# Performance work log

Hardware: AMD Instinct MI355X
Metric: run time of the kernel (lower is better)

## Reference

```python
import jax, jax.numpy as jnp
import numpy as np

HEADS = 8


def _attn_1d(xs, w_qkv, w_proj, heads, scale):
    """xs: [N, C, L] -> [N, C, L]. 1x1 conv == channel matmul."""
    n, c, l = xs.shape
    inner = w_proj.shape[1]
    d = inner // heads
    qkv = jnp.einsum('oc,ncl->nol', w_qkv, xs)          # [N, 3*inner, L]
    q, k, v = jnp.split(qkv, 3, axis=1)                  # each [N, inner, L]
    # [N, heads, L, d]
    q = q.reshape(n, heads, d, l).transpose(0, 1, 3, 2)
    k = k.reshape(n, heads, d, l).transpose(0, 1, 3, 2)
    v = v.reshape(n, heads, d, l).transpose(0, 1, 3, 2)
    attn = jax.nn.softmax(jnp.einsum('nhid,nhjd->nhij', q, k) * scale, axis=-1)
    out = jnp.einsum('nhij,nhjd->nhid', attn, v)         # [N, heads, L, d]
    out = out.transpose(0, 1, 3, 2).reshape(n, inner, l) # [N, inner, L]
    return jnp.einsum('co,nol->ncl', w_proj, out)


def _axial(x, w_qkv, w_proj, heads, scale, axis):
    b, c, h, w = x.shape
    if axis == 'h':
        xs = x.transpose(0, 3, 1, 2).reshape(b * w, c, h)
        out = _attn_1d(xs, w_qkv, w_proj, heads, scale)
        return out.reshape(b, w, c, h).transpose(0, 2, 3, 1)
    else:
        xs = x.transpose(0, 2, 1, 3).reshape(b * h, c, w)
        out = _attn_1d(xs, w_qkv, w_proj, heads, scale)
        return out.reshape(b, h, c, w).transpose(0, 2, 1, 3)


def setup_inputs() -> dict:
    key = jax.random.key(0)
    k1, k2, k3 = jax.random.split(key, 3)
    B, C, H, W = 4, 512, 128, 128
    heads = HEADS
    head_dim = C // heads
    inner = head_dim * heads
    x = jax.random.normal(k1, (B, C, H, W), dtype=jnp.float32)
    w_qkv = jax.random.normal(k2, (inner * 3, C), dtype=jnp.float32) * 0.02
    w_proj = jax.random.normal(k3, (C, inner), dtype=jnp.float32) * 0.02
    return {"x": x, "w_qkv": w_qkv, "w_proj": w_proj}


def reference(x, w_qkv, w_proj):
    c = x.shape[1]
    head_dim = c // HEADS
    scale = head_dim ** (-0.5)
    h_out = _axial(x, w_qkv, w_proj, HEADS, scale, 'h')
    w_out = _axial(h_out, w_qkv, w_proj, HEADS, scale, 'w')
    return x + w_out
```

## Files before the change

### kernel.cpp

```cpp
#include <hip/hip_runtime.h>
#include <hip/hip_bf16.h>
#include <stdint.h>

#define B_ 4
#define S_ 128
#define CH 512

typedef __attribute__((ext_vector_type(8))) __bf16 bf16x8;
typedef __attribute__((ext_vector_type(4))) float  f32x4;
typedef __attribute__((ext_vector_type(16))) float f32x16;

__device__ __forceinline__ unsigned short f2b(float f) {
    union { float f; unsigned u; } v; v.f = f;
    unsigned r = v.u + 0x7FFFu + ((v.u >> 16) & 1u);
    return (unsigned short)(r >> 16);
}

#define GLD_LDS16(gp, lp) \
    __builtin_amdgcn_global_load_lds((const __attribute__((address_space(1))) void*)(gp), \
                                     (__attribute__((address_space(3))) void*)(lp), 16, 0, 0)

__global__ void cvt_w(const float* __restrict__ wq, const float* __restrict__ wp,
                      unsigned short* __restrict__ wqb, unsigned short* __restrict__ wpb) {
    int idx = (blockIdx.x * 256 + threadIdx.x) * 4;
    const float* s; unsigned short* d; int off;
    if (idx < 1536 * 512) { s = wq; d = wqb; off = idx; }
    else                  { s = wp; d = wpb; off = idx - 1536 * 512; }
    float4 v = *(const float4*)(s + off);
    ushort4 o; o.x = f2b(v.x); o.y = f2b(v.y); o.z = f2b(v.z); o.w = f2b(v.w);
    *(ushort4*)(d + off) = o;
}

__global__ __launch_bounds__(256) void k0_tr(const float* __restrict__ x,
                                             unsigned short* __restrict__ xb) {
    __shared__ unsigned short t[64][72];
    int bid = blockIdx.x;
    int ct = bid & 7, wt = (bid >> 3) & 1, h = (bid >> 4) & 127, b = bid >> 11;
    int tid = threadIdx.x;
    int c0 = ct * 64, w0 = wt * 64;
    const float* xp = x + ((size_t)b * CH * S_ + h) * S_;
    int wl = (tid & 15) * 4;
#pragma unroll
    for (int it = 0; it < 4; ++it) {
        int c = it * 16 + (tid >> 4);
        float4 v = *(const float4*)(xp + (size_t)(c0 + c) * (S_ * S_) + w0 + wl);
        t[wl + 0][c] = f2b(v.x);
        t[wl + 1][c] = f2b(v.y);
        t[wl + 2][c] = f2b(v.z);
        t[wl + 3][c] = f2b(v.w);
    }
    __syncthreads();
#pragma unroll
    for (int it = 0; it < 2; ++it) {
        int w = it * 32 + (tid >> 3);
        int ce = (tid & 7) * 8;
        int4 v = *(const int4*)&t[w][ce];
        size_t p = (size_t)((b * 128 + w0 + w) * 128 + h);
        *(int4*)(xb + p * 512 + c0 + ce) = v;
    }
}

template<int EPI>
__global__ __launch_bounds__(512, 2) void gemm8(
    const unsigned short* __restrict__ A,
    const unsigned short* __restrict__ Bm,
    unsigned short* __restrict__ outb,
    const float* __restrict__ xres,
    float* __restrict__ outf,
    int Mtiles)
{
    __shared__ unsigned short lds[65536];
    const int NT = 8;
    int nwg = gridDim.x;
    int wg = (blockIdx.x & 7) * (nwg >> 3) + (blockIdx.x >> 3);
    int mb = wg % Mtiles, nb = wg / Mtiles;
    int m0 = mb * 256, n0 = nb * 256;
    int tid = threadIdx.x, lane = tid & 63, wid = tid >> 6;
    int wm = wid >> 2, wn = wid & 3;

    f32x16 acc[4][2] = {};

    int l31  = lane & 31;
    int rsw  = ((lane >> 2) & 3) << 4;
    int cK[4];
#pragma unroll
    for (int ks = 0; ks < 4; ++ks)
        cK[ks] = (ks * 16 + (lane >> 5) * 8) ^ rsw;
    int arow0 = (wm * 64 + l31) * 64;
    int brow  = (wn * 32 + l31) * 64;

    int srow = tid >> 3;
    int scol = ((tid & 7) * 8) ^ (((srow >> 2) & 3) << 4);
    const unsigned short* Ab0 = A  + (size_t)(m0 + srow) * 512 + scol;
    const unsigned short* Bb0 = Bm + (size_t)(n0 + (srow >> 5) * 64 + (srow & 31)) * 512 + scol;

#define STAGE_A(kt, reg) do {                                                  \
        unsigned short* lb_ = &lds[((((kt) & 1) * 2 + (reg)) * 8192)];         \
        const unsigned short* g_ = Ab0 + (size_t)(reg) * (64 * 512) + (kt) * 64;\
        GLD_LDS16(g_,             lb_ + wid * 512);                            \
        GLD_LDS16(g_ + 128 * 512, lb_ + 4096 + wid * 512);                     \
    } while (0)
#define STAGE_B(kt, reg) do {                                                  \
        unsigned short* lb_ = &lds[32768 + ((((kt) & 1) * 2 + (reg)) * 8192)]; \
        const unsigned short* g_ = Bb0 + (size_t)(reg) * (32 * 512) + (kt) * 64;\
        GLD_LDS16(g_,             lb_ + wid * 512);                            \
        GLD_LDS16(g_ + 128 * 512, lb_ + 4096 + wid * 512);                     \
    } while (0)

    STAGE_A(0, 0); STAGE_A(0, 1); STAGE_B(0, 0); STAGE_B(0, 1);
    STAGE_A(1, 0); STAGE_B(1, 0);
    asm volatile("s_waitcnt vmcnt(4)" ::: "memory");
    __builtin_amdgcn_s_barrier();

    for (int j = 0; j < NT; ++j) {
        int db = j & 1;
        bf16x8 af[2][4];
#pragma unroll
        for (int q = 0; q < 4; ++q) {
            const int mq = q >> 1, nq = q & 1;
            int bbase = 32768 + (db * 2 + nq) * 8192 + brow;
            if (nq == 0) {
                int abase = (db * 2 + mq) * 8192 + arow0;
#pragma unroll
                for (int fr = 0; fr < 2; ++fr)
#pragma unroll
                    for (int ks = 0; ks < 4; ++ks)
                        af[fr][ks] = *(const bf16x8*)&lds[abase + fr * 2048 + cK[ks]];
            }
            bf16x8 bq[4];
#pragma unroll
            for (int ks = 0; ks < 4; ++ks)
                bq[ks] = *(const bf16x8*)&lds[bbase + cK[ks]];
            if (q == 0)      { if (j + 1 < NT) STAGE_A(j + 1, 1); }
            else if (q == 1) { if (j + 1 < NT) STAGE_B(j + 1, 1); }
            else if (q == 2) { if (j + 2 < NT) STAGE_A(j + 2, 0); }
            else {
                if (j + 2 < NT) STAGE_B(j + 2, 0);
                if (j < NT - 2) asm volatile("s_waitcnt vmcnt(4)" ::: "memory");
                else            asm volatile("s_waitcnt vmcnt(0)" ::: "memory");
            }
            __builtin_amdgcn_s_barrier();
            asm volatile("s_waitcnt lgkmcnt(0)" ::: "memory");
            __builtin_amdgcn_s_setprio(1);
#pragma unroll
            for (int ks = 0; ks < 4; ++ks)
#pragma unroll
                for (int fr = 0; fr < 2; ++fr)
                    acc[mq * 2 + fr][nq] = __builtin_amdgcn_mfma_f32_32x32x16_bf16(
                        af[fr][ks], bq[ks], acc[mq * 2 + fr][nq], 0, 0, 0);
            __builtin_amdgcn_s_setprio(0);
            __builtin_amdgcn_s_barrier();
        }
    }
#undef STAGE_A
#undef STAGE_B

#pragma unroll
    for (int mi2 = 0; mi2 < 4; ++mi2) {
#pragma unroll
        for (int qd = 0; qd < 4; ++qd) {
            int row0 = m0 + wm * 128 + mi2 * 32 + qd * 8 + ((lane >> 5) << 2);
#pragma unroll
            for (int nq = 0; nq < 2; ++nq) {
                int col = n0 + wn * 64 + nq * 32 + (lane & 31);
                int i = col & 127, sq = (col >> 7) & 127, bb = col >> 14;
                float a4[4];
#pragma unroll
                for (int r = 0; r < 4; ++r) a4[r] = acc[mi2][nq][qd * 4 + r];
                if (EPI == 0) {
                    int g = row0 >> 6, d0 = row0 & 63;
                    if (g < 16) {
                        size_t base = ((size_t)(g * 4 + bb) * 16384 + (size_t)sq * 128 + i) * 64 + d0;
                        ushort4 o;
                        o.x = f2b(a4[0]); o.y = f2b(a4[1]); o.z = f2b(a4[2]); o.w = f2b(a4[3]);
                        *(ushort4*)(outb + base) = o;
                    } else {
                        size_t base = ((size_t)(g * 4 + bb) * 8192 + (size_t)sq * 64 + d0) * 128 + i;
                        outb[base]       = f2b(a4[0]);
                        outb[base + 128] = f2b(a4[1]);
                        outb[base + 256] = f2b(a4[2]);
                        outb[base + 384] = f2b(a4[3]);
                    }
                } else if (EPI == 1) {
                    size_t p2 = ((size_t)bb * 128 + i) * 128 + sq;
                    ushort4 o;
                    o.x = f2b(a4[0]); o.y = f2b(a4[1]); o.z = f2b(a4[2]); o.w = f2b(a4[3]);
                    *(ushort4*)(outb + p2 * 512 + row0) = o;
                } else {
                    size_t base = (((size_t)bb * 512 + row0) * 128 + sq) * 128 + i;
#pragma unroll
                    for (int r = 0; r < 4; ++r) {
                        size_t a_ = base + (size_t)r * 16384;
                        outf[a_] = xres[a_] + a4[r];
                    }
                }
            }
        }
    }
}

__global__ __launch_bounds__(256) void attn_k(const unsigned short* __restrict__ qkv,
                                              unsigned short* __restrict__ o2) {
    __shared__ unsigned short Qs[128 * 80];
    __shared__ unsigned short Ks[128 * 80];
    __shared__ unsigned short Vt[64 * 144];
    int bid = blockIdx.x;
    int t = bid & 7, sq = (bid >> 3) & 127, b = bid >> 10;
    int tid = threadIdx.x, lane = tid & 63, wv = tid >> 6;
    const unsigned short* qg = qkv + ((size_t)(t * 4 + b) * 16384 + (size_t)sq * 128) * 64;
    const unsigned short* kg = qkv + ((size_t)((8 + t) * 4 + b) * 16384 + (size_t)sq * 128) * 64;
    const unsigned short* vg = qkv + ((size_t)((16 + t) * 4 + b) * 8192 + (size_t)sq * 64) * 128;
    {
        int r = tid >> 3, d0 = (tid & 7) * 8;
#pragma unroll
        for (int it = 0; it < 4; ++it) {
            *(int4*)(Qs + (it * 32 + r) * 80 + d0) = *(const int4*)(qg + (it * 32 + r) * 64 + d0);
            *(int4*)(Ks + (it * 32 + r) * 80 + d0) = *(const int4*)(kg + (it * 32 + r) * 64 + d0);
        }
        int r2 = tid >> 4, i0 = (tid & 15) * 8;
#pragma unroll
        for (int it = 0; it < 4; ++it)
            *(int4*)(Vt + (it * 16 + r2) * 144 + i0) = *(const int4*)(vg + (it * 16 + r2) * 128 + i0);
    }
    __syncthreads();

    f32x4 st[8][2] = {};
#pragma unroll
    for (int kk = 0; kk < 2; ++kk) {
        int ko = kk * 32 + (lane >> 4) * 8;
        bf16x8 bq[2];
#pragma unroll
        for (int nt = 0; nt < 2; ++nt)
            bq[nt] = *(const bf16x8*)(Qs + (wv * 32 + nt * 16 + (lane & 15)) * 80 + ko);
#pragma unroll
        for (int mt = 0; mt < 8; ++mt) {
            bf16x8 ak = *(const bf16x8*)(Ks + (mt * 16 + (lane & 15)) * 80 + ko);
#pragma unroll
            for (int nt = 0; nt < 2; ++nt)
                st[mt][nt] = __builtin_amdgcn_mfma_f32_16x16x32_bf16(ak, bq[nt], st[mt][nt], 0, 0, 0);
        }
    }

    const float sc = 0.125f * 1.44269504088896f;
    float mx[2], rinv[2];
    unsigned ppk[8][2][2];
#pragma unroll
    for (int nt = 0; nt < 2; ++nt) {
        float m = -3.0e38f;
#pragma unroll
        for (int mt = 0; mt < 8; ++mt)
#pragma unroll
            for (int r = 0; r < 4; ++r)
                m = fmaxf(m, st[mt][nt][r]);
        m = fmaxf(m, __shfl_xor(m, 16));
        m = fmaxf(m, __shfl_xor(m, 32));
        mx[nt] = m * sc;
    }
#pragma unroll
    for (int nt = 0; nt < 2; ++nt) {
        float s = 0.f;
#pragma unroll
        for (int mt = 0; mt < 8; ++mt) {
            float p0 = exp2f(st[mt][nt][0] * sc - mx[nt]);
            float p1 = exp2f(st[mt][nt][1] * sc - mx[nt]);
            float p2 = exp2f(st[mt][nt][2] * sc - mx[nt]);
            float p3 = exp2f(st[mt][nt][3] * sc - mx[nt]);
            s += (p0 + p1) + (p2 + p3);
            ppk[mt][nt][0] = (unsigned)f2b(p0) | ((unsigned)f2b(p1) << 16);
            ppk[mt][nt][1] = (unsigned)f2b(p2) | ((unsigned)f2b(p3) << 16);
        }
        s += __shfl_xor(s, 16);
        s += __shfl_xor(s, 32);
        rinv[nt] = 1.0f / s;
    }

    f32x4 ov[4][2] = {};
    int g = lane >> 4;
    int ls0 = (lane & 15) | ((g & 1) << 5);
    int ls1 = ls0 | 16;
    int hi = g >> 1;
#pragma unroll
    for (int kt = 0; kt < 4; ++kt) {
        bf16x8 bp[2];
#pragma unroll
        for (int nt = 0; nt < 2; ++nt) {
            unsigned a0 = (unsigned)__shfl((int)ppk[2 * kt    ][nt][0], ls0);
            unsigned b0 = (unsigned)__shfl((int)ppk[2 * kt + 1][nt][0], ls0);
            unsigned a1 = (unsigned)__shfl((int)ppk[2 * kt    ][nt][1], ls0);
            unsigned b1 = (unsigned)__shfl((int)ppk[2 * kt + 1][nt][1], ls0);
            unsigned a2 = (unsigned)__shfl((int)ppk[2 * kt    ][nt][0], ls1);
            unsigned b2 = (unsigned)__shfl((int)ppk[2 * kt + 1][nt][0], ls1);
            unsigned a3 = (unsigned)__shfl((int)ppk[2 * kt    ][nt][1], ls1);
            unsigned b3 = (unsigned)__shfl((int)ppk[2 * kt + 1][nt][1], ls1);
            union { unsigned u[4]; bf16x8 v; } pk;
            pk.u[0] = hi ? b0 : a0;
            pk.u[1] = hi ? b1 : a1;
            pk.u[2] = hi ? b2 : a2;
            pk.u[3] = hi ? b3 : a3;
            bp[nt] = pk.v;
        }
#pragma unroll
        for (int dt = 0; dt < 4; ++dt) {
            bf16x8 av = *(const bf16x8*)(Vt + (dt * 16 + (lane & 15)) * 144 + kt * 32 + (lane >> 4) * 8);
#pragma unroll
            for (int nt = 0; nt < 2; ++nt)
                ov[dt][nt] = __builtin_amdgcn_mfma_f32_16x16x32_bf16(av, bp[nt], ov[dt][nt], 0, 0, 0);
        }
    }

#pragma unroll
    for (int dt = 0; dt < 4; ++dt) {
        int d0 = dt * 16 + (lane >> 4) * 4;
#pragma unroll
        for (int nt = 0; nt < 2; ++nt) {
            int i = wv * 32 + nt * 16 + (lane & 15);
            size_t p = ((size_t)(b * 128 + sq)) * 128 + i;
            ushort4 o;
            o.x = f2b(ov[dt][nt][0] * rinv[nt]);
            o.y = f2b(ov[dt][nt][1] * rinv[nt]);
            o.z = f2b(ov[dt][nt][2] * rinv[nt]);
            o.w = f2b(ov[dt][nt][3] * rinv[nt]);
            *(ushort4*)(o2 + p * 512 + t * 64 + d0) = o;
        }
    }
}

extern "C" void kernel_launch(void* const* d_in, const int* in_sizes, int n_in,
                              void* d_out, int out_size, void* d_ws, size_t ws_size,
                              hipStream_t stream) {
    const float* x  = (const float*)d_in[0];
    const float* wq = (const float*)d_in[1];
    const float* wp = (const float*)d_in[2];
    float* out = (float*)d_out;
    char* ws = (char*)d_ws;
    unsigned short* wqb = (unsigned short*)(ws);
    unsigned short* wpb = (unsigned short*)(ws + ((size_t)2 << 20));
    unsigned short* xb  = (unsigned short*)(ws + ((size_t)4 << 20));
    unsigned short* o2  = (unsigned short*)(ws + ((size_t)68 << 20));
    unsigned short* qkv = (unsigned short*)(ws + ((size_t)132 << 20));

    cvt_w<<<1024, 256, 0, stream>>>(wq, wp, wqb, wpb);
    k0_tr<<<8192, 256, 0, stream>>>(x, xb);
    gemm8<0><<<6 * 256, 512, 0, stream>>>(wqb, xb, qkv, nullptr, nullptr, 6);
    attn_k<<<4096, 256, 0, stream>>>(qkv, o2);
    gemm8<1><<<2 * 256, 512, 0, stream>>>(wpb, o2, xb, nullptr, nullptr, 2);
    gemm8<0><<<6 * 256, 512, 0, stream>>>(wqb, xb, qkv, nullptr, nullptr, 6);
    attn_k<<<4096, 256, 0, stream>>>(qkv, o2);
    gemm8<2><<<2 * 256, 512, 0, stream>>>(wpb, o2, nullptr, x, out, 2);
}
```

Before: 589.2 us.

## Reschedule GEMM main loop quadrants to cut barriers and reorder B staging

Restructures the inner K-loop of the bf16 MFMA GEMM so each iteration walks the four quadrants in a snake order (00,01,11,10), reusing loaded A/B fragments across adjacent quadrants. It also changes which B half is prefetched when, and drops the per-quadrant barrier pairs and explicit lgkmcnt waits. The goal is to reduce synchronisation and LDS reload overhead and overlap the global-to-LDS prefetch with MFMA work better. Correctness now depends on the new staging order avoiding overwriting LDS buffers that other waves are still reading, and without explicit lgkmcnt waits it relies on the compiler to insert them.

```diff
diff --git a/kernel.cpp b/kernel.cpp
--- a/kernel.cpp
+++ b/kernel.cpp
@@ -107,51 +107,61 @@
         GLD_LDS16(g_ + 128 * 512, lb_ + 4096 + wid * 512);                     \
     } while (0)
 
+#define LOAD_AF(reg) do {                                                      \
+        int abase_ = (db * 2 + (reg)) * 8192 + arow0;                          \
+        _Pragma("unroll")                                                      \
+        for (int fr = 0; fr < 2; ++fr)                                         \
+            _Pragma("unroll")                                                  \
+            for (int ks = 0; ks < 4; ++ks)                                     \
+                af[fr][ks] = *(const bf16x8*)&lds[abase_ + fr * 2048 + cK[ks]];\
+    } while (0)
+#define LOAD_BQ(reg) do {                                                      \
+        int bbase_ = 32768 + (db * 2 + (reg)) * 8192 + brow;                   \
+        _Pragma("unroll")                                                      \
+        for (int ks = 0; ks < 4; ++ks)                                         \
+            bq[ks] = *(const bf16x8*)&lds[bbase_ + cK[ks]];                    \
+    } while (0)
+#define MFMA8(mq, nq)                                                          \
+    __builtin_amdgcn_s_setprio(1);                                             \
+    _Pragma("unroll")                                                          \
+    for (int ks = 0; ks < 4; ++ks)                                             \
+        _Pragma("unroll")                                                      \
+        for (int fr = 0; fr < 2; ++fr)                                         \
+            acc[(mq) * 2 + fr][nq] = __builtin_amdgcn_mfma_f32_32x32x16_bf16(  \
+                af[fr][ks], bq[ks], acc[(mq) * 2 + fr][nq], 0, 0, 0);          \
+    __builtin_amdgcn_s_setprio(0);
+
     STAGE_A(0, 0); STAGE_A(0, 1); STAGE_B(0, 0); STAGE_B(0, 1);
-    STAGE_A(1, 0); STAGE_B(1, 0);
+    STAGE_A(1, 0); STAGE_B(1, 1);
     asm volatile("s_waitcnt vmcnt(4)" ::: "memory");
     __builtin_amdgcn_s_barrier();
 
     for (int j = 0; j < NT; ++j) {
-        int db = j & 1;
-        bf16x8 af[2][4];
-#pragma unroll
-        for (int q = 0; q < 4; ++q) {
-            const int mq = q >> 1, nq = q & 1;
-            int bbase = 32768 + (db * 2 + nq) * 8192 + brow;
-            if (nq == 0) {
-                int abase = (db * 2 + mq) * 8192 + arow0;
-#pragma unroll
-                for (int fr = 0; fr < 2; ++fr)
-#pragma unroll
-                    for (int ks = 0; ks < 4; ++ks)
-                        af[fr][ks] = *(const bf16x8*)&lds[abase + fr * 2048 + cK[ks]];
-            }
-            bf16x8 bq[4];
-#pragma unroll
-            for (int ks = 0; ks < 4; ++ks)
-                bq[ks] = *(const bf16x8*)&lds[bbase + cK[ks]];
-            if (q == 0)      { if (j + 1 < NT) STAGE_A(j + 1, 1); }
-            else if (q == 1) { if (j + 1 < NT) STAGE_B(j + 1, 1); }
-            else if (q == 2) { if (j + 2 < NT) STAGE_A(j + 2, 0); }
-            else {
-                if (j + 2 < NT) STAGE_B(j + 2, 0);
-                if (j < NT - 2) asm volatile("s_waitcnt vmcnt(4)" ::: "memory");
-                else            asm volatile("s_waitcnt vmcnt(0)" ::: "memory");
-            }
-            __builtin_amdgcn_s_barrier();
-            asm volatile("s_waitcnt lgkmcnt(0)" ::: "memory");
-            __builtin_amdgcn_s_setprio(1);
-#pragma unroll
-            for (int ks = 0; ks < 4; ++ks)
-#pragma unroll
-                for (int fr = 0; fr < 2; ++fr)
-                    acc[mq * 2 + fr][nq] = __builtin_amdgcn_mfma_f32_32x32x16_bf16(
-                        af[fr][ks], bq[ks], acc[mq * 2 + fr][nq], 0, 0, 0);
-            __builtin_amdgcn_s_setprio(0);
-            __builtin_amdgcn_s_barrier();
-        }
-    }
+        const int db = j & 1;
+        bf16x8 af[2][4], bq[4];
+        LOAD_AF(0);
+        LOAD_BQ(0);
+        if (j + 1 < NT) STAGE_A(j + 1, 1);
+        MFMA8(0, 0)
+        LOAD_BQ(1);
+        if (j + 1 < NT) STAGE_B(j + 1, 0);
+        MFMA8(0, 1)
+        __builtin_amdgcn_s_barrier();
+        LOAD_AF(1);
+        LOAD_BQ(1);
+        if (j + 2 < NT) STAGE_A(j + 2, 0);
+        MFMA8(1, 1)
+        __builtin_amdgcn_s_barrier();
+        LOAD_BQ(0);
+        if (j + 2 < NT) STAGE_B(j + 2, 1);
+        MFMA8(1, 0)
+        if (j < NT - 2)       asm volatile("s_waitcnt vmcnt(4)" ::: "memory");
+        else if (j == NT - 2) asm volatile("s_waitcnt vmcnt(0)" ::: "memory");
+        __builtin_amdgcn_s_barrier();
+    }
+#undef MFMA8
+#undef LOAD_BQ
+#undef LOAD_AF
 #undef STAGE_A
 #undef STAGE_B
 
```

New measurement: 581.6 us. No clear change (-1.3%).

## Restructure GEMM main loop to triple-buffered BK=32 pipeline with one barrier per step

Applied to the files above, without the earlier changes.

Replaces the double-buffered BK=64 loop, which had four quarter-steps each separated by barriers, with a three-slot ring of BK=32 tiles. Each iteration prefetches the tile two steps ahead, loads all A/B fragments, issues 16 MFMAs, then waits and hits a single barrier. The LDS swizzle and staging addressing are rewritten to match the 32-wide rows, and LDS use drops to 96KB. The aim is fewer barriers and better overlap of global loads with MFMA, at the cost of twice as many loop iterations and a new swizzle scheme that could add bank conflicts.

```diff
diff --git a/kernel.cpp b/kernel.cpp
--- a/kernel.cpp
+++ b/kernel.cpp
@@ -69,8 +69,8 @@
     float* __restrict__ outf,
     int Mtiles)
 {
-    __shared__ unsigned short lds[65536];
-    const int NT = 8;
+    __shared__ unsigned short lds[49152];
+    const int NT = 16;
     int nwg = gridDim.x;
     int wg = (blockIdx.x & 7) * (nwg >> 3) + (blockIdx.x >> 3);
     int mb = wg % Mtiles, nb = wg / Mtiles;
@@ -81,79 +81,63 @@
     f32x16 acc[4][2] = {};
 
     int l31  = lane & 31;
-    int rsw  = ((lane >> 2) & 3) << 4;
-    int cK[4];
-#pragma unroll
-    for (int ks = 0; ks < 4; ++ks)
-        cK[ks] = (ks * 16 + (lane >> 5) * 8) ^ rsw;
-    int arow0 = (wm * 64 + l31) * 64;
-    int brow  = (wn * 32 + l31) * 64;
-
-    int srow = tid >> 3;
-    int scol = ((tid & 7) * 8) ^ (((srow >> 2) & 3) << 4);
-    const unsigned short* Ab0 = A  + (size_t)(m0 + srow) * 512 + scol;
-    const unsigned short* Bb0 = Bm + (size_t)(n0 + (srow >> 5) * 64 + (srow & 31)) * 512 + scol;
-
-#define STAGE_A(kt, reg) do {                                                  \
-        unsigned short* lb_ = &lds[((((kt) & 1) * 2 + (reg)) * 8192)];         \
-        const unsigned short* g_ = Ab0 + (size_t)(reg) * (64 * 512) + (kt) * 64;\
-        GLD_LDS16(g_,             lb_ + wid * 512);                            \
-        GLD_LDS16(g_ + 128 * 512, lb_ + 4096 + wid * 512);                     \
+    int ck[2];
+#pragma unroll
+    for (int ks = 0; ks < 2; ++ks)
+        ck[ks] = (((ks * 2 + (lane >> 5)) ^ (lane & 3)) << 3);
+    int arow = (wm * 128 + l31) * 32;
+    int brow = (wn * 64 + l31) * 32;
+
+    int dchunk = (lane & 3) ^ ((lane >> 2) & 3);
+    const unsigned short* Asrc = A  + (size_t)(m0 + 16 * wid + (lane >> 2)) * 512 + dchunk * 8;
+    const unsigned short* Bsrc = Bm + (size_t)(n0 + 16 * wid + (lane >> 2)) * 512 + dchunk * 8;
+
+#define STAGE(buf, kt) do {                                                    \
+        unsigned short* la_ = &lds[(buf) * 16384 + 16 * wid * 32];             \
+        unsigned short* lb_ = la_ + 8192;                                      \
+        GLD_LDS16(Asrc + (kt) * 32,             la_);                          \
+        GLD_LDS16(Asrc + 128 * 512 + (kt) * 32, la_ + 4096);                   \
+        GLD_LDS16(Bsrc + (kt) * 32,             lb_);                          \
+        GLD_LDS16(Bsrc + 128 * 512 + (kt) * 32, lb_ + 4096);                   \
     } while (0)
-#define STAGE_B(kt, reg) do {                                                  \
-        unsigned short* lb_ = &lds[32768 + ((((kt) & 1) * 2 + (reg)) * 8192)]; \
-        const unsigned short* g_ = Bb0 + (size_t)(reg) * (32 * 512) + (kt) * 64;\
-        GLD_LDS16(g_,             lb_ + wid * 512);                            \
-        GLD_LDS16(g_ + 128 * 512, lb_ + 4096 + wid * 512);                     \
-    } while (0)
-
-    STAGE_A(0, 0); STAGE_A(0, 1); STAGE_B(0, 0); STAGE_B(0, 1);
-    STAGE_A(1, 0); STAGE_B(1, 0);
+
+    STAGE(0, 0); STAGE(1, 1);
     asm volatile("s_waitcnt vmcnt(4)" ::: "memory");
     __builtin_amdgcn_s_barrier();
 
     for (int j = 0; j < NT; ++j) {
-        int db = j & 1;
-        bf16x8 af[2][4];
-#pragma unroll
-        for (int q = 0; q < 4; ++q) {
-            const int mq = q >> 1, nq = q & 1;
-            int bbase = 32768 + (db * 2 + nq) * 8192 + brow;
-            if (nq == 0) {
-                int abase = (db * 2 + mq) * 8192 + arow0;
-#pragma unroll
-                for (int fr = 0; fr < 2; ++fr)
-#pragma unroll
-                    for (int ks = 0; ks < 4; ++ks)
-                        af[fr][ks] = *(const bf16x8*)&lds[abase + fr * 2048 + cK[ks]];
-            }
-            bf16x8 bq[4];
-#pragma unroll
-            for (int ks = 0; ks < 4; ++ks)
-                bq[ks] = *(const bf16x8*)&lds[bbase + cK[ks]];
-            if (q == 0)      { if (j + 1 < NT) STAGE_A(j + 1, 1); }
-            else if (q == 1) { if (j + 1 < NT) STAGE_B(j + 1, 1); }
-            else if (q == 2) { if (j + 2 < NT) STAGE_A(j + 2, 0); }
-            else {
-                if (j + 2 < NT) STAGE_B(j + 2, 0);
-                if (j < NT - 2) asm volatile("s_waitcnt vmcnt(4)" ::: "memory");
-                else            asm volatile("s_waitcnt vmcnt(0)" ::: "memory");
-            }
-            __builtin_amdgcn_s_barrier();
-            asm volatile("s_waitcnt lgkmcnt(0)" ::: "memory");
-            __builtin_amdgcn_s_setprio(1);
-#pragma unroll
-            for (int ks = 0; ks < 4; ++ks)
-#pragma unroll
-                for (int fr = 0; fr < 2; ++fr)
-                    acc[mq * 2 + fr][nq] = __builtin_amdgcn_mfma_f32_32x32x16_bf16(
-                        af[fr][ks], bq[ks], acc[mq * 2 + fr][nq], 0, 0, 0);
-            __builtin_amdgcn_s_setprio(0);
-            __builtin_amdgcn_s_barrier();
-        }
-    }
-#undef STAGE_A
-#undef STAGE_B
+        const int buf = j % 3;
+        if (j + 2 < NT) STAGE((j + 2) % 3, j + 2);
+        bf16x8 af[4][2], bq[2][2];
+        {
+            int ab = buf * 16384 + arow;
+#pragma unroll
+            for (int mq = 0; mq < 4; ++mq)
+#pragma unroll
+                for (int ks = 0; ks < 2; ++ks)
+                    af[mq][ks] = *(const bf16x8*)&lds[ab + mq * 1024 + ck[ks]];
+            int bb = buf * 16384 + 8192 + brow;
+#pragma unroll
+            for (int nq = 0; nq < 2; ++nq)
+#pragma unroll
+                for (int ks = 0; ks < 2; ++ks)
+                    bq[nq][ks] = *(const bf16x8*)&lds[bb + nq * 1024 + ck[ks]];
+        }
+        __builtin_amdgcn_s_setprio(1);
+#pragma unroll
+        for (int ks = 0; ks < 2; ++ks)
+#pragma unroll
+            for (int mq = 0; mq < 4; ++mq)
+#pragma unroll
+                for (int nq = 0; nq < 2; ++nq)
+                    acc[mq][nq] = __builtin_amdgcn_mfma_f32_32x32x16_bf16(
+                        af[mq][ks], bq[nq][ks], acc[mq][nq], 0, 0, 0);
+        __builtin_amdgcn_s_setprio(0);
+        if (j + 2 < NT)      asm volatile("s_waitcnt vmcnt(4)" ::: "memory");
+        else if (j == NT - 2) asm volatile("s_waitcnt vmcnt(0)" ::: "memory");
+        if (j < NT - 1) __builtin_amdgcn_s_barrier();
+    }
+#undef STAGE
 
 #pragma unroll
     for (int mi2 = 0; mi2 < 4; ++mi2) {
```

After: 639.0 us. 8.5% more time.
